# Kernel optimization log

Measured on AMD Instinct MI355X. Metric: run time of the kernel, lower is better.

Reference implementation:

```python
import jax, jax.numpy as jnp
import numpy as np

S, N, D, F, L = 16, 64, 1270, 150, 8  # sentences, entities, emb dim, ffnn_size, num_labels


def _xavier(key, shape):
    lim = np.sqrt(6.0 / (shape[0] + shape[1])).astype(np.float32)
    return jax.random.uniform(key, shape, jnp.float32, -lim, lim)


def setup_inputs() -> dict:
    key = jax.random.key(0)
    ks = jax.random.split(key, 8)
    entity_emb = jax.random.normal(ks[0], (S, N, D), jnp.float32)
    entity_scores = jax.random.normal(ks[1], (S, N), jnp.float32)
    rel_labels = jax.random.randint(ks[2], (S, N, N), 0, L)
    num_predicted_entities = jax.random.randint(ks[3], (S,), 0, N)
    # Linear params stored [in, out] (y = x @ W + b), transpose of torch layout.
    W_in = _xavier(ks[4], (3 * D, F))
    b_in = jnp.zeros((F,), jnp.float32)
    W_h = _xavier(ks[5], (F, F))
    b_h = jnp.zeros((F,), jnp.float32)
    W_out = _xavier(ks[6], (F, L - 1))
    b_out = jnp.zeros((L - 1,), jnp.float32)
    return {
        "entity_emb": entity_emb,
        "entity_scores": entity_scores,
        "W_in": W_in, "b_in": b_in,
        "W_h": W_h, "b_h": b_h,
        "W_out": W_out, "b_out": b_out,
        "rel_labels": rel_labels,
        "num_predicted_entities": num_predicted_entities,
    }


def reference(entity_emb, entity_scores, W_in, b_in, W_h, b_h, W_out, b_out,
              rel_labels, num_predicted_entities):
    s, n, d = entity_emb.shape
    # pair_emb = concat([e1_tiled, e2_tiled, e1*e2]) @ W_in  ==  split-weight fused form
    # (avoids materializing the [S,N,N,3D] tensor; same math).
    W1, W2, W3 = W_in[:d], W_in[d:2 * d], W_in[2 * d:]
    h = (jnp.einsum('sid,df->sif', entity_emb, W1)[:, :, None, :]
         + jnp.einsum('sjd,df->sjf', entity_emb, W2)[:, None, :, :]
         + jnp.einsum('sid,sjd,df->sijf', entity_emb, entity_emb, W3)
         + b_in)  # [S,N,N,F]
    # NOTE: original applies two more Linear layers with NO nonlinearity between them.
    h = h @ W_h + b_h
    scores = h @ W_out + b_out  # [S,N,N,L-1]
    # dropout is identity at inference (reference baseline)
    rel = scores + entity_scores[:, :, None, None] + entity_scores[:, None, :, None]
    dummy = jnp.zeros((s, n, n, 1), rel.dtype)
    rel_scores = jnp.concatenate([dummy, rel], axis=3)  # [S,N,N,L]
    # per-element cross entropy (reduction='none'), then pair mask, then sum
    logp = jax.nn.log_softmax(rel_scores, axis=-1)
    ce = -jnp.take_along_axis(logp, rel_labels[..., None], axis=-1)[..., 0]  # [S,N,N]
    ent_mask = jnp.arange(n)[None, :] < num_predicted_entities[:, None]  # [S,N]
    pair_mask = ent_mask[:, :, None] & ent_mask[:, None, :]  # [S,N,N]
    loss = jnp.sum(jnp.where(pair_mask, ce, jnp.zeros((), ce.dtype)))
    return rel_scores, loss
```

## Files before the change

### kernel.cpp

```cpp
#include <hip/hip_runtime.h>
#include <hip/hip_bf16.h>
#include <stdint.h>

typedef __attribute__((ext_vector_type(8))) short bf16x8;
typedef __attribute__((ext_vector_type(16))) float f32x16;

#define S_ 16
#define N_ 64
#define D_ 1270
#define F_ 150
#define KP_ 1280
#define FP_ 160
#define NKT 80
#define LOSS_OFF (S_*N_*N_*8)

#define HSTR 172

__device__ inline short f2b(float x) {
    union { float f; uint32_t u; } v; v.f = x;
    uint32_t r = (v.u + 0x7fffu + ((v.u >> 16) & 1u)) >> 16;
    return (short)r;
}
__device__ inline bf16x8 as_bf16x8(uint4 u) {
    union { uint4 a; bf16x8 b; } c; c.a = u; return c.b;
}

__global__ void k_pack(const float* __restrict__ emb, const float* __restrict__ win,
                       const float* __restrict__ wh, const float* __restrict__ wout,
                       short* __restrict__ eapk, short* __restrict__ w3pk,
                       short* __restrict__ w12pk, short* __restrict__ whpk,
                       short* __restrict__ wopk, float* __restrict__ out) {
    int t = blockIdx.x * 256 + threadIdx.x;
    if (t == 0) out[LOSS_OFF] = 0.f;
    const int TOT_EA = S_ * NKT * 2 * 64;
    const int NW3 = NKT * 5 * 64, NW12 = NKT * 10 * 64, NWH = 10 * 5 * 64, NWO = 10 * 64;
    if (t < TOT_EA) {
        int l  = t & 63;
        int mt = (t >> 6) & 1;
        int kt = (t >> 7) % NKT;
        int s  = t / (NKT * 2 * 64);
        int i  = (l & 31) + mt * 32;
        int k0 = kt * 16 + (l >> 5) * 8;
        const float* src = emb + (size_t)(s * N_ + i) * D_;
        bf16x8 pk;
        if (k0 + 8 <= D_) {
            float2 v0 = *(const float2*)(src + k0);
            float2 v1 = *(const float2*)(src + k0 + 2);
            float2 v2 = *(const float2*)(src + k0 + 4);
            float2 v3 = *(const float2*)(src + k0 + 6);
            pk[0]=f2b(v0.x); pk[1]=f2b(v0.y); pk[2]=f2b(v1.x); pk[3]=f2b(v1.y);
            pk[4]=f2b(v2.x); pk[5]=f2b(v2.y); pk[6]=f2b(v3.x); pk[7]=f2b(v3.y);
        } else {
            #pragma unroll
            for (int u = 0; u < 8; ++u) {
                int k = k0 + u;
                pk[u] = (k < D_) ? f2b(src[k]) : (short)0;
            }
        }
        *(bf16x8*)(eapk + (size_t)t * 8) = pk;
        return;
    }
    int t0 = t - TOT_EA;
    if (t0 < NW3) {
        int l = t0 & 63, nt = (t0 >> 6) % 5, kt = t0 / 320;
        int k0 = kt * 16 + (l >> 5) * 8, f = (l & 31) + nt * 32;
        bf16x8 pk;
        #pragma unroll
        for (int u = 0; u < 8; ++u) {
            int k = k0 + u;
            pk[u] = (k < D_ && f < F_) ? f2b(win[((size_t)(2 * D_) + k) * F_ + f]) : (short)0;
        }
        *(bf16x8*)(w3pk + (size_t)t0 * 8) = pk;
    } else if (t0 < NW3 + NW12) {
        int t2 = t0 - NW3;
        int l = t2 & 63, nt = (t2 >> 6) % 10, kt = t2 / 640;
        int k0 = kt * 16 + (l >> 5) * 8, c = (l & 31) + nt * 32;
        bf16x8 pk;
        #pragma unroll
        for (int u = 0; u < 8; ++u) {
            int k = k0 + u;
            float val = 0.f;
            if (k < D_) {
                if (c < FP_) { if (c < F_) val = win[(size_t)k * F_ + c]; }
                else { int f = c - FP_; if (f < F_) val = win[((size_t)D_ + k) * F_ + f]; }
            }
            pk[u] = f2b(val);
        }
        *(bf16x8*)(w12pk + (size_t)t2 * 8) = pk;
    } else if (t0 < NW3 + NW12 + NWH) {
        int t3 = t0 - NW3 - NW12;
        int l = t3 & 63, nt = (t3 >> 6) % 5, kt = t3 / 320;
        int k0 = kt * 16 + (l >> 5) * 8, f = (l & 31) + nt * 32;
        bf16x8 pk;
        #pragma unroll
        for (int u = 0; u < 8; ++u) {
            int k = k0 + u;
            pk[u] = (k < F_ && f < F_) ? f2b(wh[(size_t)k * F_ + f]) : (short)0;
        }
        *(bf16x8*)(whpk + (size_t)t3 * 8) = pk;
    } else if (t0 < NW3 + NW12 + NWH + NWO) {
        int t4 = t0 - NW3 - NW12 - NWH;
        int l = t4 & 63, kt = t4 >> 6;
        int k0 = kt * 16 + (l >> 5) * 8, f = l & 31;
        bf16x8 pk;
        #pragma unroll
        for (int u = 0; u < 8; ++u) {
            int k = k0 + u;
            pk[u] = (k < F_ && f < 7) ? f2b(wout[k * 7 + f]) : (short)0;
        }
        *(bf16x8*)(wopk + (size_t)t4 * 8) = pk;
    }
}

__global__ __launch_bounds__(128) void k_p12(const short* __restrict__ eapk,
                                             const short* __restrict__ w12pk,
                                             const float* __restrict__ bin,
                                             float* __restrict__ p1, float* __restrict__ p2) {
    __shared__ float red[16][64];
    int bid = blockIdx.x;
    int x = bid & 7, k = bid >> 3;
    int s = x * 2 + (k / 20);
    int rr = k % 20;
    int nt = rr >> 1, mt = rr & 1;
    int lane = threadIdx.x & 63, ks = threadIdx.x >> 6;
    f32x16 acc;
    #pragma unroll
    for (int r = 0; r < 16; ++r) acc[r] = 0.f;
    const size_t abase = (size_t)s * NKT * 2 * 64 * 8;
    #pragma unroll 8
    for (int kt = ks * 40; kt < ks * 40 + 40; ++kt) {
        bf16x8 a = *(const bf16x8*)(eapk + abase + ((size_t)kt * 2 + mt) * 64 * 8 + (size_t)lane * 8);
        bf16x8 b = *(const bf16x8*)(w12pk + ((size_t)(kt * 10 + nt) * 64 + lane) * 8);
        acc = __builtin_amdgcn_mfma_f32_32x32x16_bf16(a, b, acc, 0, 0, 0);
    }
    if (ks == 1) {
        #pragma unroll
        for (int r = 0; r < 16; ++r) red[r][lane] = acc[r];
    }
    __syncthreads();
    if (ks == 0) {
        int c = (lane & 31) + nt * 32;
        #pragma unroll
        for (int r = 0; r < 16; ++r) {
            float v = acc[r] + red[r][lane];
            int i = (r & 3) + 8 * (r >> 2) + 4 * (lane >> 5) + mt * 32;
            if (c < FP_) {
                p1[(size_t)(s * N_ + i) * FP_ + c] = v;
            } else {
                int f = c - FP_;
                float bv = (f < F_) ? bin[f] : 0.f;
                p2[(size_t)(s * N_ + i) * FP_ + f] = v + bv;
            }
        }
    }
}

template<int NB>
__device__ __forceinline__ void run_gemm1(const char* ea, const char* w3,
                                          const float* ej0, const float* ej1,
                                          f32x16 (&acc)[2][3]) {
    uint4 euA, euB;
    uint4 bfA[3], bfB[3];
    float4 ejA[4], ejB[4];

    auto fetch = [&](int kt, uint4& eu, uint4 (&bfv)[3], float4 (&ejr)[4]) {
        eu = *(const uint4*)(ea + (size_t)kt * 2048);
        #pragma unroll
        for (int nb = 0; nb < NB; ++nb)
            bfv[nb] = *(const uint4*)(w3 + (size_t)kt * 5120 + nb * 1024);
        ejr[0] = *(const float4*)(ej0 + kt * 16);
        ejr[1] = *(const float4*)(ej0 + kt * 16 + 4);
        ejr[2] = *(const float4*)(ej1 + kt * 16);
        ejr[3] = *(const float4*)(ej1 + kt * 16 + 4);
    };
    auto step = [&](const uint4& eu, const uint4 (&bfv)[3], const float4 (&ejr)[4]) {
        float ev0[8] = {ejr[0].x,ejr[0].y,ejr[0].z,ejr[0].w,ejr[1].x,ejr[1].y,ejr[1].z,ejr[1].w};
        float ev1[8] = {ejr[2].x,ejr[2].y,ejr[2].z,ejr[2].w,ejr[3].x,ejr[3].y,ejr[3].z,ejr[3].w};
        uint32_t ew[4] = {eu.x, eu.y, eu.z, eu.w};
        union { uint32_t u[4]; bf16x8 v; } av0, av1;
        #pragma unroll
        for (int p = 0; p < 4; ++p) {
            float elo = __uint_as_float(ew[p] << 16);
            float ehi = __uint_as_float(ew[p] & 0xffff0000u);
            float f00 = elo * ev0[2*p], f01 = ehi * ev0[2*p+1];
            float f10 = elo * ev1[2*p], f11 = ehi * ev1[2*p+1];
            uint32_t p0, p1v;
            asm("v_cvt_pk_bf16_f32 %0, %1, %2" : "=v"(p0)  : "v"(f00), "v"(f01));
            asm("v_cvt_pk_bf16_f32 %0, %1, %2" : "=v"(p1v) : "v"(f10), "v"(f11));
            av0.u[p] = p0; av1.u[p] = p1v;
        }
        #pragma unroll
        for (int nb = 0; nb < NB; ++nb) {
            bf16x8 bb = as_bf16x8(bfv[nb]);
            acc[0][nb] = __builtin_amdgcn_mfma_f32_32x32x16_bf16(av0.v, bb, acc[0][nb], 0, 0, 0);
            acc[1][nb] = __builtin_amdgcn_mfma_f32_32x32x16_bf16(av1.v, bb, acc[1][nb], 0, 0, 0);
        }
    };

    fetch(0, euA, bfA, ejA);
    fetch(1, euB, bfB, ejB);
    #pragma unroll 1
    for (int kt = 0; kt < NKT; kt += 2) {
        step(euA, bfA, ejA);
        if (kt + 2 < NKT) fetch(kt + 2, euA, bfA, ejA);
        step(euB, bfB, ejB);
        if (kt + 3 < NKT) fetch(kt + 3, euB, bfB, ejB);
    }
}

template<int NB, int NT0>
__device__ __forceinline__ void write_h(const f32x16 (&acc)[2][3], short* hB,
                                        const float* p1s, const float* p2r0,
                                        const float* p2r1, int lane, int mt) {
    #pragma unroll
    for (int nb = 0; nb < NB; ++nb) {
        const int f = (lane & 31) + (NT0 + nb) * 32;
        float p1v[16];
        #pragma unroll
        for (int r = 0; r < 16; ++r) {
            int i = (r & 3) + 8 * (r >> 2) + 4 * (lane >> 5) + mt * 32;
            p1v[r] = p1s[(size_t)i * FP_ + f];
        }
        const float p20 = p2r0[f], p21 = p2r1[f];
        #pragma unroll
        for (int r = 0; r < 16; ++r) {
            int i = (r & 3) + 8 * (r >> 2) + 4 * (lane >> 5) + mt * 32;
            hB[i * HSTR + f]             = f2b(acc[0][nb][r] + p1v[r] + p20);
            hB[64 * HSTR + i * HSTR + f] = f2b(acc[1][nb][r] + p1v[r] + p21);
        }
    }
}

__global__ __launch_bounds__(256, 1) void k_main(
    const float* __restrict__ emb, const float* __restrict__ esc,
    const short* __restrict__ eapk, const short* __restrict__ w3pk,
    const short* __restrict__ whpk, const short* __restrict__ wopk,
    const float* __restrict__ p1g, const float* __restrict__ p2g,
    const float* __restrict__ bhv, const float* __restrict__ bout,
    const int* __restrict__ labels, const int* __restrict__ nump,
    float* __restrict__ out) {

    __shared__ char lds[48128];
    float* sbuf = (float*)lds;
    float* ejB  = (float*)(lds + 4096);
    short* hB   = (short*)(lds + 4096);

    const int tid = threadIdx.x, lane = tid & 63, w = tid >> 6;
    const int mt = w & 1, nh = w >> 1;
    const int hi8 = (lane >> 5) << 3;
    const int bid = blockIdx.x;
    const int x = bid & 7, kk2 = bid >> 3;
    const int s = x * 2 + (kk2 >> 5);
    const int j0 = (kk2 & 31) * 2;

    for (int idx = tid; idx < 2 * KP_; idx += 256) {
        int jr = idx / KP_, k = idx - jr * KP_;
        ejB[idx] = (k < D_) ? emb[(size_t)(s * N_ + j0 + jr) * D_ + k] : 0.f;
    }
    __syncthreads();

    f32x16 acc[2][3];
    #pragma unroll
    for (int jl = 0; jl < 2; ++jl)
        #pragma unroll
        for (int nb = 0; nb < 3; ++nb)
            #pragma unroll
            for (int r = 0; r < 16; ++r) acc[jl][nb][r] = 0.f;

    {
        const char* ea = (const char*)eapk + (size_t)s * 163840 + mt * 1024 + lane * 16;
        const char* w3 = (const char*)w3pk + (nh ? 3 : 0) * 1024 + lane * 16;
        const float* ej0 = ejB + hi8;
        const float* ej1 = ej0 + KP_;
        if (nh == 0) run_gemm1<3>(ea, w3, ej0, ej1, acc);
        else         run_gemm1<2>(ea, w3, ej0, ej1, acc);
    }
    __syncthreads();

    {
        const float* p1s = p1g + (size_t)(s * N_) * FP_;
        const float* p2r0 = p2g + (size_t)(s * N_ + j0) * FP_;
        const float* p2r1 = p2r0 + FP_;
        if (nh == 0) write_h<3, 0>(acc, hB, p1s, p2r0, p2r1, lane, mt);
        else         write_h<2, 3>(acc, hB, p1s, p2r0, p2r1, lane, mt);
    }
    __syncthreads();

    f32x16 acc2[5];
    #pragma unroll
    for (int c = 0; c < 5; ++c)
        #pragma unroll
        for (int r = 0; r < 16; ++r) acc2[c][r] = 0.f;
    #pragma unroll 1
    for (int kt = 0; kt < 10; ++kt) {
        #pragma unroll
        for (int c = 0; c < 5; ++c) {
            int t = w + 4 * c;
            int jl2 = t / 10, tt = t % 10;
            int mt2 = tt / 5, nt2 = tt % 5;
            const short* ap = hB + jl2 * (64 * HSTR) + ((lane & 31) + mt2 * 32) * HSTR
                            + kt * 16 + hi8;
            short4 alo = *(const short4*)ap;
            short4 ahi = *(const short4*)(ap + 4);
            union { short sh[8]; bf16x8 v; } av;
            av.sh[0] = alo.x; av.sh[1] = alo.y; av.sh[2] = alo.z; av.sh[3] = alo.w;
            av.sh[4] = ahi.x; av.sh[5] = ahi.y; av.sh[6] = ahi.z; av.sh[7] = ahi.w;
            bf16x8 b = *(const bf16x8*)(whpk + ((size_t)(kt * 5 + nt2) * 64 + lane) * 8);
            acc2[c] = __builtin_amdgcn_mfma_f32_32x32x16_bf16(av.v, b, acc2[c], 0, 0, 0);
        }
    }
    __syncthreads();

    #pragma unroll
    for (int c = 0; c < 5; ++c) {
        int t = w + 4 * c;
        int jl2 = t / 10, tt = t % 10;
        int mt2 = tt / 5, nt2 = tt % 5;
        int f = (lane & 31) + nt2 * 32;
        float bhf = (f < F_) ? bhv[f] : 0.f;
        #pragma unroll
        for (int r = 0; r < 16; ++r) {
            int i = (r & 3) + 8 * (r >> 2) + 4 * (lane >> 5) + mt2 * 32;
            short hv = (f < F_) ? f2b(acc2[c][r] + bhf) : (short)0;
            hB[jl2 * (64 * HSTR) + i * HSTR + f] = hv;
        }
    }
    __syncthreads();

    {
        int jl3 = w >> 1, mt3 = w & 1;
        f32x16 acc3;
        #pragma unroll
        for (int r = 0; r < 16; ++r) acc3[r] = 0.f;
        #pragma unroll 1
        for (int kt = 0; kt < 10; ++kt) {
            const short* ap = hB + jl3 * (64 * HSTR) + ((lane & 31) + mt3 * 32) * HSTR
                            + kt * 16 + hi8;
            short4 alo = *(const short4*)ap;
            short4 ahi = *(const short4*)(ap + 4);
            union { short sh[8]; bf16x8 v; } av;
            av.sh[0] = alo.x; av.sh[1] = alo.y; av.sh[2] = alo.z; av.sh[3] = alo.w;
            av.sh[4] = ahi.x; av.sh[5] = ahi.y; av.sh[6] = ahi.z; av.sh[7] = ahi.w;
            bf16x8 b = *(const bf16x8*)(wopk + ((size_t)(kt * 64) + lane) * 8);
            acc3 = __builtin_amdgcn_mfma_f32_32x32x16_bf16(av.v, b, acc3, 0, 0, 0);
        }
        int c3 = lane & 31;
        if (c3 < 7) {
            float bo = bout[c3];
            #pragma unroll
            for (int r = 0; r < 16; ++r) {
                int i = (r & 3) + 8 * (r >> 2) + 4 * (lane >> 5) + mt3 * 32;
                sbuf[jl3 * 512 + i * 8 + c3] = acc3[r] + bo;
            }
        }
    }
    __syncthreads();

    if (tid < 128) {
        int jl = tid >> 6;
        int i = tid & 63;
        int j = j0 + jl;
        const float esi = esc[s * N_ + i];
        const float esj = esc[s * N_ + j];
        float rr[8];
        rr[0] = 0.f;
        #pragma unroll
        for (int l = 1; l < 8; ++l) rr[l] = sbuf[jl * 512 + i * 8 + (l - 1)] + esi + esj;

        float4* op = (float4*)(out + ((size_t)(s * N_ + i) * N_ + j) * 8);
        op[0] = make_float4(rr[0], rr[1], rr[2], rr[3]);
        op[1] = make_float4(rr[4], rr[5], rr[6], rr[7]);

        float m = rr[0];
        #pragma unroll
        for (int l = 1; l < 8; ++l) m = fmaxf(m, rr[l]);
        float sum = 0.f;
        #pragma unroll
        for (int l = 0; l < 8; ++l) sum += expf(rr[l] - m);
        const float lse = m + logf(sum);

        const int lab = labels[(s * N_ + i) * N_ + j];
        float ce = lse - rr[lab];
        const int np = nump[s];
        float v = (i < np && j < np) ? ce : 0.f;
        #pragma unroll
        for (int off = 32; off; off >>= 1) v += __shfl_down(v, off);
        if ((tid & 63) == 0) atomicAdd(out + LOSS_OFF, v);
    }
}

extern "C" void kernel_launch(void* const* d_in, const int* in_sizes, int n_in,
                              void* d_out, int out_size, void* d_ws, size_t ws_size,
                              hipStream_t stream) {
    const float* emb    = (const float*)d_in[0];
    const float* esc    = (const float*)d_in[1];
    const float* Win    = (const float*)d_in[2];
    const float* bin    = (const float*)d_in[3];
    const float* Wh     = (const float*)d_in[4];
    const float* bh     = (const float*)d_in[5];
    const float* Wout   = (const float*)d_in[6];
    const float* bout   = (const float*)d_in[7];
    const int*   labels = (const int*)d_in[8];
    const int*   nump   = (const int*)d_in[9];
    float* out = (float*)d_out;

    char* ws = (char*)d_ws;
    short* eapk  = (short*)(ws);
    short* w3pk  = (short*)(ws + 2621440);
    short* w12pk = (short*)(ws + 3031040);
    short* whpk  = (short*)(ws + 3850240);
    short* wopk  = (short*)(ws + 3901440);
    float* p1    = (float*)(ws + 3911680);
    float* p2    = (float*)(ws + 4567040);

    const int TOT_EA = S_ * NKT * 2 * 64;
    const int NW = NKT * 5 * 64 + NKT * 10 * 64 + 10 * 5 * 64 + 10 * 64;
    k_pack<<<(TOT_EA + NW + 255) / 256, 256, 0, stream>>>(emb, Win, Wh, Wout,
                                                          eapk, w3pk, w12pk, whpk, wopk, out);
    k_p12<<<320, 128, 0, stream>>>(eapk, w12pk, bin, p1, p2);
    k_main<<<S_ * 32, 256, 0, stream>>>(emb, esc, eapk, w3pk, whpk, wopk, p1, p2,
                                        bh, bout, labels, nump, out);
}
```

Measured before the change: 83.51 us.

## Split fused main kernel into GEMM1 phase and Wh/Wout/loss phase via global buffer

Splits the monolithic k_main into two kernels. The first computes the pairwise first-layer hidden tensor and writes it as bf16 to a 20 MB workspace buffer. The second runs the Wh and Wout GEMMs plus the log-softmax loss, using twice as many blocks without the single-occupancy bound. The aim is to lift the occupancy and latency limits of the fused tail stage, at the cost of an extra global round trip of the hidden tensor and one more launch. It falls back to the old kernel if the workspace is too small.

Result: slower. 101.7 us (+21.8%).

```diff
diff --git a/kernel.cpp b/kernel.cpp
--- a/kernel.cpp
+++ b/kernel.cpp
@@ -161,7 +161,7 @@
                                           f32x16 (&acc)[2][3]) {
     uint4 euA, euB;
     uint4 bfA[3], bfB[3];
-    float4 ejA[4], ejB[4];
+    float4 ejA[4], ejB4[4];
 
     auto fetch = [&](int kt, uint4& eu, uint4 (&bfv)[3], float4 (&ejr)[4]) {
         eu = *(const uint4*)(ea + (size_t)kt * 2048);
@@ -198,13 +198,13 @@
     };
 
     fetch(0, euA, bfA, ejA);
-    fetch(1, euB, bfB, ejB);
+    fetch(1, euB, bfB, ejB4);
     #pragma unroll 1
     for (int kt = 0; kt < NKT; kt += 2) {
         step(euA, bfA, ejA);
         if (kt + 2 < NKT) fetch(kt + 2, euA, bfA, ejA);
-        step(euB, bfB, ejB);
-        if (kt + 3 < NKT) fetch(kt + 3, euB, bfB, ejB);
+        step(euB, bfB, ejB4);
+        if (kt + 3 < NKT) fetch(kt + 3, euB, bfB, ejB4);
     }
 }
 
@@ -228,6 +228,180 @@
             hB[i * HSTR + f]             = f2b(acc[0][nb][r] + p1v[r] + p20);
             hB[64 * HSTR + i * HSTR + f] = f2b(acc[1][nb][r] + p1v[r] + p21);
         }
+    }
+}
+
+__global__ __launch_bounds__(256, 1) void k_phase1(
+    const float* __restrict__ emb,
+    const short* __restrict__ eapk, const short* __restrict__ w3pk,
+    const float* __restrict__ p1g, const float* __restrict__ p2g,
+    short* __restrict__ hg) {
+
+    __shared__ char lds[44032];
+    float* ejB = (float*)lds;
+    short* hB  = (short*)lds;
+
+    const int tid = threadIdx.x, lane = tid & 63, w = tid >> 6;
+    const int mt = w & 1, nh = w >> 1;
+    const int hi8 = (lane >> 5) << 3;
+    const int bid = blockIdx.x;
+    const int x = bid & 7, kk2 = bid >> 3;
+    const int s = x * 2 + (kk2 >> 5);
+    const int j0 = (kk2 & 31) * 2;
+
+    for (int idx = tid; idx < 2 * KP_; idx += 256) {
+        int jr = idx / KP_, k = idx - jr * KP_;
+        ejB[idx] = (k < D_) ? emb[(size_t)(s * N_ + j0 + jr) * D_ + k] : 0.f;
+    }
+    __syncthreads();
+
+    f32x16 acc[2][3];
+    #pragma unroll
+    for (int jl = 0; jl < 2; ++jl)
+        #pragma unroll
+        for (int nb = 0; nb < 3; ++nb)
+            #pragma unroll
+            for (int r = 0; r < 16; ++r) acc[jl][nb][r] = 0.f;
+
+    {
+        const char* ea = (const char*)eapk + (size_t)s * 163840 + mt * 1024 + lane * 16;
+        const char* w3 = (const char*)w3pk + (nh ? 3 : 0) * 1024 + lane * 16;
+        const float* ej0 = ejB + hi8;
+        const float* ej1 = ej0 + KP_;
+        if (nh == 0) run_gemm1<3>(ea, w3, ej0, ej1, acc);
+        else         run_gemm1<2>(ea, w3, ej0, ej1, acc);
+    }
+    __syncthreads();
+
+    {
+        const float* p1s = p1g + (size_t)(s * N_) * FP_;
+        const float* p2r0 = p2g + (size_t)(s * N_ + j0) * FP_;
+        const float* p2r1 = p2r0 + FP_;
+        if (nh == 0) write_h<3, 0>(acc, hB, p1s, p2r0, p2r1, lane, mt);
+        else         write_h<2, 3>(acc, hB, p1s, p2r0, p2r1, lane, mt);
+    }
+    __syncthreads();
+
+    for (int idx = tid; idx < 2 * 64 * 40; idx += 256) {
+        int jl = idx / 2560;
+        int rem = idx - jl * 2560;
+        int row = rem / 40, c8 = rem - row * 40;
+        *(short4*)(hg + (((size_t)(s * 64 + j0 + jl) * 64 + row) * 160) + c8 * 4)
+            = *(const short4*)(hB + jl * (64 * HSTR) + row * HSTR + c8 * 4);
+    }
+}
+
+__global__ __launch_bounds__(256) void k_phase2(
+    const short* __restrict__ hg, const short* __restrict__ whpk,
+    const short* __restrict__ wopk, const float* __restrict__ esc,
+    const float* __restrict__ bhv, const float* __restrict__ bout,
+    const int* __restrict__ labels, const int* __restrict__ nump,
+    float* __restrict__ out) {
+
+    __shared__ char lds[24064];
+    short* h2B  = (short*)lds;
+    float* sbuf = (float*)(lds + 22016);
+
+    const int tid = threadIdx.x, lane = tid & 63, w = tid >> 6;
+    const int hi8 = (lane >> 5) << 3;
+    const int bid = blockIdx.x;
+    const int x = bid & 7, r2 = bid >> 3;
+    const int s = x * 2 + (r2 >> 6);
+    const int j = r2 & 63;
+
+    const short* hrow = hg + (size_t)(s * 64 + j) * 64 * 160;
+
+    f32x16 acc2[3];
+    #pragma unroll
+    for (int c = 0; c < 3; ++c)
+        #pragma unroll
+        for (int r = 0; r < 16; ++r) acc2[c][r] = 0.f;
+    #pragma unroll 1
+    for (int kt = 0; kt < 10; ++kt) {
+        #pragma unroll
+        for (int c = 0; c < 3; ++c) {
+            int t = w + 4 * c;
+            if (t >= 10) break;
+            int mt2 = t / 5, nt2 = t % 5;
+            int i = (lane & 31) + mt2 * 32;
+            bf16x8 a = *(const bf16x8*)(hrow + i * 160 + kt * 16 + hi8);
+            bf16x8 b = *(const bf16x8*)(whpk + ((size_t)(kt * 5 + nt2) * 64 + lane) * 8);
+            acc2[c] = __builtin_amdgcn_mfma_f32_32x32x16_bf16(a, b, acc2[c], 0, 0, 0);
+        }
+    }
+
+    #pragma unroll
+    for (int c = 0; c < 3; ++c) {
+        int t = w + 4 * c;
+        if (t >= 10) break;
+        int mt2 = t / 5, nt2 = t % 5;
+        int f = (lane & 31) + nt2 * 32;
+        float bhf = (f < F_) ? bhv[f] : 0.f;
+        #pragma unroll
+        for (int r = 0; r < 16; ++r) {
+            int i = (r & 3) + 8 * (r >> 2) + 4 * (lane >> 5) + mt2 * 32;
+            short hv = (f < F_) ? f2b(acc2[c][r] + bhf) : (short)0;
+            h2B[i * HSTR + f] = hv;
+        }
+    }
+    __syncthreads();
+
+    if (w < 2) {
+        int mt3 = w;
+        f32x16 acc3;
+        #pragma unroll
+        for (int r = 0; r < 16; ++r) acc3[r] = 0.f;
+        #pragma unroll 1
+        for (int kt = 0; kt < 10; ++kt) {
+            const short* ap = h2B + ((lane & 31) + mt3 * 32) * HSTR + kt * 16 + hi8;
+            short4 alo = *(const short4*)ap;
+            short4 ahi = *(const short4*)(ap + 4);
+            union { short sh[8]; bf16x8 v; } av;
+            av.sh[0] = alo.x; av.sh[1] = alo.y; av.sh[2] = alo.z; av.sh[3] = alo.w;
+            av.sh[4] = ahi.x; av.sh[5] = ahi.y; av.sh[6] = ahi.z; av.sh[7] = ahi.w;
+            bf16x8 b = *(const bf16x8*)(wopk + ((size_t)(kt * 64) + lane) * 8);
+            acc3 = __builtin_amdgcn_mfma_f32_32x32x16_bf16(av.v, b, acc3, 0, 0, 0);
+        }
+        int c3 = lane & 31;
+        if (c3 < 7) {
+            float bo = bout[c3];
+            #pragma unroll
+            for (int r = 0; r < 16; ++r) {
+                int i = (r & 3) + 8 * (r >> 2) + 4 * (lane >> 5) + mt3 * 32;
+                sbuf[i * 8 + c3] = acc3[r] + bo;
+            }
+        }
+    }
+    __syncthreads();
+
+    if (tid < 64) {
+        int i = tid;
+        const float esi = esc[s * N_ + i];
+        const float esj = esc[s * N_ + j];
+        float rr[8];
+        rr[0] = 0.f;
+        #pragma unroll
+        for (int l = 1; l < 8; ++l) rr[l] = sbuf[i * 8 + (l - 1)] + esi + esj;
+
+        float4* op = (float4*)(out + ((size_t)(s * N_ + i) * N_ + j) * 8);
+        op[0] = make_float4(rr[0], rr[1], rr[2], rr[3]);
+        op[1] = make_float4(rr[4], rr[5], rr[6], rr[7]);
+
+        float m = rr[0];
+        #pragma unroll
+        for (int l = 1; l < 8; ++l) m = fmaxf(m, rr[l]);
+        float sum = 0.f;
+        #pragma unroll
+        for (int l = 0; l < 8; ++l) sum += expf(rr[l] - m);
+        const float lse = m + logf(sum);
+
+        const int lab = labels[(s * N_ + i) * N_ + j];
+        float ce = lse - rr[lab];
+        const int np = nump[s];
+        float v = (i < np && j < np) ? ce : 0.f;
+        #pragma unroll
+        for (int off = 32; off; off >>= 1) v += __shfl_down(v, off);
+        if (tid == 0) atomicAdd(out + LOSS_OFF, v);
     }
 }
 
@@ -412,12 +586,21 @@
     short* wopk  = (short*)(ws + 3901440);
     float* p1    = (float*)(ws + 3911680);
     float* p2    = (float*)(ws + 4567040);
+    const size_t HG_OFF = 5222400;
+    short* hg    = (short*)(ws + HG_OFF);
 
     const int TOT_EA = S_ * NKT * 2 * 64;
     const int NW = NKT * 5 * 64 + NKT * 10 * 64 + 10 * 5 * 64 + 10 * 64;
     k_pack<<<(TOT_EA + NW + 255) / 256, 256, 0, stream>>>(emb, Win, Wh, Wout,
                                                           eapk, w3pk, w12pk, whpk, wopk, out);
     k_p12<<<320, 128, 0, stream>>>(eapk, w12pk, bin, p1, p2);
-    k_main<<<S_ * 32, 256, 0, stream>>>(emb, esc, eapk, w3pk, whpk, wopk, p1, p2,
-                                        bh, bout, labels, nump, out);
-}
+
+    if (ws_size >= HG_OFF + 20971520ull) {
+        k_phase1<<<S_ * 32, 256, 0, stream>>>(emb, eapk, w3pk, p1, p2, hg);
+        k_phase2<<<S_ * 64, 256, 0, stream>>>(hg, whpk, wopk, esc, bh, bout,
+                                              labels, nump, out);
+    } else {
+        k_main<<<S_ * 32, 256, 0, stream>>>(emb, esc, eapk, w3pk, whpk, wopk, p1, p2,
+                                            bh, bout, labels, nump, out);
+    }
+}
```

## Split the two j columns across waves, doubling k_main to 512 threads

Applied to the files above, without the earlier changes.

The main kernel now launches 8 waves per block instead of 4. Each wave handles one j column of the pair-product GEMM rather than both, which halves the per-wave accumulators and the scale/convert work. The second and third GEMM stages redistribute their tiles over 8 waves, leaving some idle. The goal is more latency hiding and less register pressure per wave, but each wave now re-reads the shared E and W3 operands, roughly doubling the global/L2 traffic for those operands.

New measurement: 84.02 us, median of 2. Within noise of the previous version (+0.6%).

```diff
diff --git a/kernel.cpp b/kernel.cpp
--- a/kernel.cpp
+++ b/kernel.cpp
@@ -157,81 +157,64 @@
 
 template<int NB>
 __device__ __forceinline__ void run_gemm1(const char* ea, const char* w3,
-                                          const float* ej0, const float* ej1,
-                                          f32x16 (&acc)[2][3]) {
+                                          const float* ej0, f32x16 (&acc)[3]) {
     uint4 euA, euB;
     uint4 bfA[3], bfB[3];
-    float4 ejA[4], ejB[4];
-
-    auto fetch = [&](int kt, uint4& eu, uint4 (&bfv)[3], float4 (&ejr)[4]) {
+    float4 ejA[2], ejB4[2];
+
+    auto fetch = [&](int kt, uint4& eu, uint4 (&bfv)[3], float4 (&ejr)[2]) {
         eu = *(const uint4*)(ea + (size_t)kt * 2048);
         #pragma unroll
         for (int nb = 0; nb < NB; ++nb)
             bfv[nb] = *(const uint4*)(w3 + (size_t)kt * 5120 + nb * 1024);
         ejr[0] = *(const float4*)(ej0 + kt * 16);
         ejr[1] = *(const float4*)(ej0 + kt * 16 + 4);
-        ejr[2] = *(const float4*)(ej1 + kt * 16);
-        ejr[3] = *(const float4*)(ej1 + kt * 16 + 4);
     };
-    auto step = [&](const uint4& eu, const uint4 (&bfv)[3], const float4 (&ejr)[4]) {
-        float ev0[8] = {ejr[0].x,ejr[0].y,ejr[0].z,ejr[0].w,ejr[1].x,ejr[1].y,ejr[1].z,ejr[1].w};
-        float ev1[8] = {ejr[2].x,ejr[2].y,ejr[2].z,ejr[2].w,ejr[3].x,ejr[3].y,ejr[3].z,ejr[3].w};
+    auto step = [&](const uint4& eu, const uint4 (&bfv)[3], const float4 (&ejr)[2]) {
+        float ev[8] = {ejr[0].x,ejr[0].y,ejr[0].z,ejr[0].w,ejr[1].x,ejr[1].y,ejr[1].z,ejr[1].w};
         uint32_t ew[4] = {eu.x, eu.y, eu.z, eu.w};
-        union { uint32_t u[4]; bf16x8 v; } av0, av1;
+        union { uint32_t u[4]; bf16x8 v; } av;
         #pragma unroll
         for (int p = 0; p < 4; ++p) {
-            float elo = __uint_as_float(ew[p] << 16);
-            float ehi = __uint_as_float(ew[p] & 0xffff0000u);
-            float f00 = elo * ev0[2*p], f01 = ehi * ev0[2*p+1];
-            float f10 = elo * ev1[2*p], f11 = ehi * ev1[2*p+1];
-            uint32_t p0, p1v;
-            asm("v_cvt_pk_bf16_f32 %0, %1, %2" : "=v"(p0)  : "v"(f00), "v"(f01));
-            asm("v_cvt_pk_bf16_f32 %0, %1, %2" : "=v"(p1v) : "v"(f10), "v"(f11));
-            av0.u[p] = p0; av1.u[p] = p1v;
-        }
-        #pragma unroll
-        for (int nb = 0; nb < NB; ++nb) {
-            bf16x8 bb = as_bf16x8(bfv[nb]);
-            acc[0][nb] = __builtin_amdgcn_mfma_f32_32x32x16_bf16(av0.v, bb, acc[0][nb], 0, 0, 0);
-            acc[1][nb] = __builtin_amdgcn_mfma_f32_32x32x16_bf16(av1.v, bb, acc[1][nb], 0, 0, 0);
-        }
+            float flo = __uint_as_float(ew[p] << 16) * ev[2 * p];
+            float fhi = __uint_as_float(ew[p] & 0xffff0000u) * ev[2 * p + 1];
+            uint32_t pk;
+            asm("v_cvt_pk_bf16_f32 %0, %1, %2" : "=v"(pk) : "v"(flo), "v"(fhi));
+            av.u[p] = pk;
+        }
+        #pragma unroll
+        for (int nb = 0; nb < NB; ++nb)
+            acc[nb] = __builtin_amdgcn_mfma_f32_32x32x16_bf16(av.v, as_bf16x8(bfv[nb]), acc[nb], 0, 0, 0);
     };
 
     fetch(0, euA, bfA, ejA);
-    fetch(1, euB, bfB, ejB);
+    fetch(1, euB, bfB, ejB4);
     #pragma unroll 1
     for (int kt = 0; kt < NKT; kt += 2) {
         step(euA, bfA, ejA);
         if (kt + 2 < NKT) fetch(kt + 2, euA, bfA, ejA);
-        step(euB, bfB, ejB);
-        if (kt + 3 < NKT) fetch(kt + 3, euB, bfB, ejB);
+        step(euB, bfB, ejB4);
+        if (kt + 3 < NKT) fetch(kt + 3, euB, bfB, ejB4);
     }
 }
 
 template<int NB, int NT0>
-__device__ __forceinline__ void write_h(const f32x16 (&acc)[2][3], short* hB,
-                                        const float* p1s, const float* p2r0,
-                                        const float* p2r1, int lane, int mt) {
+__device__ __forceinline__ void write_h1(const f32x16 (&acc)[3], short* hBj,
+                                         const float* p1s, const float* p2r,
+                                         int lane, int mt) {
     #pragma unroll
     for (int nb = 0; nb < NB; ++nb) {
         const int f = (lane & 31) + (NT0 + nb) * 32;
-        float p1v[16];
+        const float p2v = p2r[f];
         #pragma unroll
         for (int r = 0; r < 16; ++r) {
             int i = (r & 3) + 8 * (r >> 2) + 4 * (lane >> 5) + mt * 32;
-            p1v[r] = p1s[(size_t)i * FP_ + f];
-        }
-        const float p20 = p2r0[f], p21 = p2r1[f];
-        #pragma unroll
-        for (int r = 0; r < 16; ++r) {
-            int i = (r & 3) + 8 * (r >> 2) + 4 * (lane >> 5) + mt * 32;
-            hB[i * HSTR + f]             = f2b(acc[0][nb][r] + p1v[r] + p20);
-            hB[64 * HSTR + i * HSTR + f] = f2b(acc[1][nb][r] + p1v[r] + p21);
-        }
-    }
-}
-
-__global__ __launch_bounds__(256, 1) void k_main(
+            hBj[i * HSTR + f] = f2b(acc[nb][r] + p1s[(size_t)i * FP_ + f] + p2v);
+        }
+    }
+}
+
+__global__ __launch_bounds__(512, 1) void k_main(
     const float* __restrict__ emb, const float* __restrict__ esc,
     const short* __restrict__ eapk, const short* __restrict__ w3pk,
     const short* __restrict__ whpk, const short* __restrict__ wopk,
@@ -246,56 +229,54 @@
     short* hB   = (short*)(lds + 4096);
 
     const int tid = threadIdx.x, lane = tid & 63, w = tid >> 6;
-    const int mt = w & 1, nh = w >> 1;
+    const int jl = w & 1, mt = (w >> 1) & 1, nh = w >> 2;
     const int hi8 = (lane >> 5) << 3;
     const int bid = blockIdx.x;
     const int x = bid & 7, kk2 = bid >> 3;
     const int s = x * 2 + (kk2 >> 5);
     const int j0 = (kk2 & 31) * 2;
 
-    for (int idx = tid; idx < 2 * KP_; idx += 256) {
+    for (int idx = tid; idx < 2 * KP_; idx += 512) {
         int jr = idx / KP_, k = idx - jr * KP_;
         ejB[idx] = (k < D_) ? emb[(size_t)(s * N_ + j0 + jr) * D_ + k] : 0.f;
     }
     __syncthreads();
 
-    f32x16 acc[2][3];
+    f32x16 acc[3];
     #pragma unroll
-    for (int jl = 0; jl < 2; ++jl)
-        #pragma unroll
-        for (int nb = 0; nb < 3; ++nb)
-            #pragma unroll
-            for (int r = 0; r < 16; ++r) acc[jl][nb][r] = 0.f;
+    for (int nb = 0; nb < 3; ++nb)
+        #pragma unroll
+        for (int r = 0; r < 16; ++r) acc[nb][r] = 0.f;
 
     {
         const char* ea = (const char*)eapk + (size_t)s * 163840 + mt * 1024 + lane * 16;
         const char* w3 = (const char*)w3pk + (nh ? 3 : 0) * 1024 + lane * 16;
-        const float* ej0 = ejB + hi8;
-        const float* ej1 = ej0 + KP_;
-        if (nh == 0) run_gemm1<3>(ea, w3, ej0, ej1, acc);
-        else         run_gemm1<2>(ea, w3, ej0, ej1, acc);
+        const float* ej0 = ejB + jl * KP_ + hi8;
+        if (nh == 0) run_gemm1<3>(ea, w3, ej0, acc);
+        else         run_gemm1<2>(ea, w3, ej0, acc);
     }
     __syncthreads();
 
     {
         const float* p1s = p1g + (size_t)(s * N_) * FP_;
-        const float* p2r0 = p2g + (size_t)(s * N_ + j0) * FP_;
-        const float* p2r1 = p2r0 + FP_;
-        if (nh == 0) write_h<3, 0>(acc, hB, p1s, p2r0, p2r1, lane, mt);
-        else         write_h<2, 3>(acc, hB, p1s, p2r0, p2r1, lane, mt);
-    }
-    __syncthreads();
-
-    f32x16 acc2[5];
+        const float* p2r = p2g + (size_t)(s * N_ + j0 + jl) * FP_;
+        short* hBj = hB + jl * (64 * HSTR);
+        if (nh == 0) write_h1<3, 0>(acc, hBj, p1s, p2r, lane, mt);
+        else         write_h1<2, 3>(acc, hBj, p1s, p2r, lane, mt);
+    }
+    __syncthreads();
+
+    f32x16 acc2[3];
     #pragma unroll
-    for (int c = 0; c < 5; ++c)
+    for (int c = 0; c < 3; ++c)
         #pragma unroll
         for (int r = 0; r < 16; ++r) acc2[c][r] = 0.f;
     #pragma unroll 1
     for (int kt = 0; kt < 10; ++kt) {
         #pragma unroll
-        for (int c = 0; c < 5; ++c) {
-            int t = w + 4 * c;
+        for (int c = 0; c < 3; ++c) {
+            int t = w + 8 * c;
+            if (t >= 20) break;
             int jl2 = t / 10, tt = t % 10;
             int mt2 = tt / 5, nt2 = tt % 5;
             const short* ap = hB + jl2 * (64 * HSTR) + ((lane & 31) + mt2 * 32) * HSTR
@@ -312,8 +293,9 @@
     __syncthreads();
 
     #pragma unroll
-    for (int c = 0; c < 5; ++c) {
-        int t = w + 4 * c;
+    for (int c = 0; c < 3; ++c) {
+        int t = w + 8 * c;
+        if (t >= 20) break;
         int jl2 = t / 10, tt = t % 10;
         int mt2 = tt / 5, nt2 = tt % 5;
         int f = (lane & 31) + nt2 * 32;
@@ -327,7 +309,7 @@
     }
     __syncthreads();
 
-    {
+    if (w < 4) {
         int jl3 = w >> 1, mt3 = w & 1;
         f32x16 acc3;
         #pragma unroll
@@ -357,15 +339,15 @@
     __syncthreads();
 
     if (tid < 128) {
-        int jl = tid >> 6;
+        int jle = tid >> 6;
         int i = tid & 63;
-        int j = j0 + jl;
+        int j = j0 + jle;
         const float esi = esc[s * N_ + i];
         const float esj = esc[s * N_ + j];
         float rr[8];
         rr[0] = 0.f;
         #pragma unroll
-        for (int l = 1; l < 8; ++l) rr[l] = sbuf[jl * 512 + i * 8 + (l - 1)] + esi + esj;
+        for (int l = 1; l < 8; ++l) rr[l] = sbuf[jle * 512 + i * 8 + (l - 1)] + esi + esj;
 
         float4* op = (float4*)(out + ((size_t)(s * N_ + i) * N_ + j) * 8);
         op[0] = make_float4(rr[0], rr[1], rr[2], rr[3]);
@@ -418,6 +400,6 @@
     k_pack<<<(TOT_EA + NW + 255) / 256, 256, 0, stream>>>(emb, Win, Wh, Wout,
                                                           eapk, w3pk, w12pk, whpk, wopk, out);
     k_p12<<<320, 128, 0, stream>>>(eapk, w12pk, bin, p1, p2);
-    k_main<<<S_ * 32, 256, 0, stream>>>(emb, esc, eapk, w3pk, whpk, wopk, p1, p2,
+    k_main<<<S_ * 32, 512, 0, stream>>>(emb, esc, eapk, w3pk, whpk, wopk, p1, p2,
                                         bh, bout, labels, nump, out);
 }
```

## Split GEMM1 K-loop across two wave groups with LDS reduction

Applied to the files above, without the earlier changes.

Doubles the block to 512 threads and splits the 80-step K loop of the first GEMM into two halves handled by separate wave groups. Partial accumulators are summed through LDS in two phases before the h write. Later stages redistribute tiles over eight waves. This aims to improve latency hiding and per-block throughput of the dominant GEMM, at the cost of extra barriers, an LDS reduction pass and higher register pressure per CU.

Result: slower. 88.50 us (+6.0%).

```diff
diff --git a/kernel.cpp b/kernel.cpp
--- a/kernel.cpp
+++ b/kernel.cpp
@@ -161,7 +161,7 @@
                                           f32x16 (&acc)[2][3]) {
     uint4 euA, euB;
     uint4 bfA[3], bfB[3];
-    float4 ejA[4], ejB[4];
+    float4 ejA[4], ejB4[4];
 
     auto fetch = [&](int kt, uint4& eu, uint4 (&bfv)[3], float4 (&ejr)[4]) {
         eu = *(const uint4*)(ea + (size_t)kt * 2048);
@@ -198,13 +198,13 @@
     };
 
     fetch(0, euA, bfA, ejA);
-    fetch(1, euB, bfB, ejB);
+    fetch(1, euB, bfB, ejB4);
     #pragma unroll 1
-    for (int kt = 0; kt < NKT; kt += 2) {
+    for (int kt = 0; kt < 40; kt += 2) {
         step(euA, bfA, ejA);
-        if (kt + 2 < NKT) fetch(kt + 2, euA, bfA, ejA);
-        step(euB, bfB, ejB);
-        if (kt + 3 < NKT) fetch(kt + 3, euB, bfB, ejB);
+        if (kt + 2 < 40) fetch(kt + 2, euA, bfA, ejA);
+        step(euB, bfB, ejB4);
+        if (kt + 3 < 40) fetch(kt + 3, euB, bfB, ejB4);
     }
 }
 
@@ -231,7 +231,7 @@
     }
 }
 
-__global__ __launch_bounds__(256, 1) void k_main(
+__global__ __launch_bounds__(512, 1) void k_main(
     const float* __restrict__ emb, const float* __restrict__ esc,
     const short* __restrict__ eapk, const short* __restrict__ w3pk,
     const short* __restrict__ whpk, const short* __restrict__ wopk,
@@ -240,20 +240,21 @@
     const int* __restrict__ labels, const int* __restrict__ nump,
     float* __restrict__ out) {
 
-    __shared__ char lds[48128];
+    __shared__ char lds[49152];
     float* sbuf = (float*)lds;
     float* ejB  = (float*)(lds + 4096);
     short* hB   = (short*)(lds + 4096);
+    float* red  = (float*)lds;
 
     const int tid = threadIdx.x, lane = tid & 63, w = tid >> 6;
-    const int mt = w & 1, nh = w >> 1;
+    const int ks = w & 1, mt = (w >> 1) & 1, nh = w >> 2;
     const int hi8 = (lane >> 5) << 3;
     const int bid = blockIdx.x;
     const int x = bid & 7, kk2 = bid >> 3;
     const int s = x * 2 + (kk2 >> 5);
     const int j0 = (kk2 & 31) * 2;
 
-    for (int idx = tid; idx < 2 * KP_; idx += 256) {
+    for (int idx = tid; idx < 2 * KP_; idx += 512) {
         int jr = idx / KP_, k = idx - jr * KP_;
         ejB[idx] = (k < D_) ? emb[(size_t)(s * N_ + j0 + jr) * D_ + k] : 0.f;
     }
@@ -268,16 +269,59 @@
             for (int r = 0; r < 16; ++r) acc[jl][nb][r] = 0.f;
 
     {
-        const char* ea = (const char*)eapk + (size_t)s * 163840 + mt * 1024 + lane * 16;
-        const char* w3 = (const char*)w3pk + (nh ? 3 : 0) * 1024 + lane * 16;
-        const float* ej0 = ejB + hi8;
+        const char* ea = (const char*)eapk + (size_t)s * 163840 + (size_t)ks * 40 * 2048
+                       + mt * 1024 + lane * 16;
+        const char* w3 = (const char*)w3pk + (size_t)ks * 40 * 5120
+                       + (nh ? 3 : 0) * 1024 + lane * 16;
+        const float* ej0 = ejB + ks * 640 + hi8;
         const float* ej1 = ej0 + KP_;
         if (nh == 0) run_gemm1<3>(ea, w3, ej0, ej1, acc);
         else         run_gemm1<2>(ea, w3, ej0, ej1, acc);
     }
     __syncthreads();
 
-    {
+    if (ks == 1 && nh == 0) {
+        #pragma unroll
+        for (int jl = 0; jl < 2; ++jl)
+            #pragma unroll
+            for (int nb = 0; nb < 3; ++nb)
+                #pragma unroll
+                for (int r = 0; r < 16; ++r)
+                    red[((mt * 6 + jl * 3 + nb) * 16 + r) * 64 + lane] = acc[jl][nb][r];
+    }
+    __syncthreads();
+    if (ks == 0 && nh == 0) {
+        #pragma unroll
+        for (int jl = 0; jl < 2; ++jl)
+            #pragma unroll
+            for (int nb = 0; nb < 3; ++nb)
+                #pragma unroll
+                for (int r = 0; r < 16; ++r)
+                    acc[jl][nb][r] += red[((mt * 6 + jl * 3 + nb) * 16 + r) * 64 + lane];
+    }
+    __syncthreads();
+    if (ks == 1 && nh == 1) {
+        #pragma unroll
+        for (int jl = 0; jl < 2; ++jl)
+            #pragma unroll
+            for (int nb = 0; nb < 2; ++nb)
+                #pragma unroll
+                for (int r = 0; r < 16; ++r)
+                    red[((mt * 4 + jl * 2 + nb) * 16 + r) * 64 + lane] = acc[jl][nb][r];
+    }
+    __syncthreads();
+    if (ks == 0 && nh == 1) {
+        #pragma unroll
+        for (int jl = 0; jl < 2; ++jl)
+            #pragma unroll
+            for (int nb = 0; nb < 2; ++nb)
+                #pragma unroll
+                for (int r = 0; r < 16; ++r)
+                    acc[jl][nb][r] += red[((mt * 4 + jl * 2 + nb) * 16 + r) * 64 + lane];
+    }
+    __syncthreads();
+
+    if (ks == 0) {
         const float* p1s = p1g + (size_t)(s * N_) * FP_;
         const float* p2r0 = p2g + (size_t)(s * N_ + j0) * FP_;
         const float* p2r1 = p2r0 + FP_;
@@ -286,16 +330,17 @@
     }
     __syncthreads();
 
-    f32x16 acc2[5];
+    f32x16 acc2[3];
     #pragma unroll
-    for (int c = 0; c < 5; ++c)
+    for (int c = 0; c < 3; ++c)
         #pragma unroll
         for (int r = 0; r < 16; ++r) acc2[c][r] = 0.f;
     #pragma unroll 1
     for (int kt = 0; kt < 10; ++kt) {
         #pragma unroll
-        for (int c = 0; c < 5; ++c) {
-            int t = w + 4 * c;
+        for (int c = 0; c < 3; ++c) {
+            int t = w + 8 * c;
+            if (t >= 20) break;
             int jl2 = t / 10, tt = t % 10;
             int mt2 = tt / 5, nt2 = tt % 5;
             const short* ap = hB + jl2 * (64 * HSTR) + ((lane & 31) + mt2 * 32) * HSTR
@@ -312,8 +357,9 @@
     __syncthreads();
 
     #pragma unroll
-    for (int c = 0; c < 5; ++c) {
-        int t = w + 4 * c;
+    for (int c = 0; c < 3; ++c) {
+        int t = w + 8 * c;
+        if (t >= 20) break;
         int jl2 = t / 10, tt = t % 10;
         int mt2 = tt / 5, nt2 = tt % 5;
         int f = (lane & 31) + nt2 * 32;
@@ -327,7 +373,7 @@
     }
     __syncthreads();
 
-    {
+    if (w < 4) {
         int jl3 = w >> 1, mt3 = w & 1;
         f32x16 acc3;
         #pragma unroll
@@ -357,15 +403,15 @@
     __syncthreads();
 
     if (tid < 128) {
-        int jl = tid >> 6;
+        int jle = tid >> 6;
         int i = tid & 63;
-        int j = j0 + jl;
+        int j = j0 + jle;
         const float esi = esc[s * N_ + i];
         const float esj = esc[s * N_ + j];
         float rr[8];
         rr[0] = 0.f;
         #pragma unroll
-        for (int l = 1; l < 8; ++l) rr[l] = sbuf[jl * 512 + i * 8 + (l - 1)] + esi + esj;
+        for (int l = 1; l < 8; ++l) rr[l] = sbuf[jle * 512 + i * 8 + (l - 1)] + esi + esj;
 
         float4* op = (float4*)(out + ((size_t)(s * N_ + i) * N_ + j) * 8);
         op[0] = make_float4(rr[0], rr[1], rr[2], rr[3]);
@@ -418,6 +464,6 @@
     k_pack<<<(TOT_EA + NW + 255) / 256, 256, 0, stream>>>(emb, Win, Wh, Wout,
                                                           eapk, w3pk, w12pk, whpk, wopk, out);
     k_p12<<<320, 128, 0, stream>>>(eapk, w12pk, bin, p1, p2);
-    k_main<<<S_ * 32, 256, 0, stream>>>(emb, esc, eapk, w3pk, whpk, wopk, p1, p2,
+    k_main<<<S_ * 32, 512, 0, stream>>>(emb, esc, eapk, w3pk, whpk, wopk, p1, p2,
                                         bh, bout, labels, nump, out);
 }
```
